# Kernel tuning notes

Hardware: AMD Instinct MI355X
Metric: run time of the kernel (lower is better)

The kernel has to match this reference:

```python
import jax, jax.numpy as jnp
import numpy as np

EPS_COS = 1e-8   # torch cosine_similarity eps
EPS_DEN = 1e-6   # denominator eps in original loss
TEMP = 0.1


def setup_inputs() -> dict:
    key = jax.random.key(0)
    k1, _ = jax.random.split(key)
    N, D = 16384, 2048
    x = jax.random.normal(k1, (N, D), dtype=jnp.float32)
    pos_pair = jnp.arange(2, dtype=jnp.int64)  # (i, j) = (0, 1), i != j
    return {"x": x, "pos_pair": pos_pair}


def reference(x, pos_pair):
    # x: [N, D]; pos_pair: [2] int indices (i, j)
    i = pos_pair[0]
    j = pos_pair[1]
    xi = x[i]                                        # [D] anchor
    # cosine similarity of anchor against every row (single fused matvec)
    dots = x @ xi                                    # [N]
    norms = jnp.maximum(jnp.linalg.norm(x, axis=1), EPS_COS)   # [N]
    ni = jnp.maximum(jnp.linalg.norm(xi), EPS_COS)
    cos = dots / (norms * ni)                        # [N]
    e = jnp.exp(cos / TEMP)                          # [N]
    # denominator sums over all k != i (k == j included, as in original)
    mask = jnp.arange(x.shape[0]) != i
    denominator = jnp.sum(jnp.where(mask, e, 0.0))
    nominator = e[j]
    loss = -jnp.log(nominator / (denominator + EPS_DEN))
    return loss.reshape(1)  # original returns shape [1]
```

## Files before the change

kernel.cpp:

```cpp
#include <hip/hip_runtime.h>
#include <math.h>

#define D 2048
#define EPS_COS 1e-8f
#define EPS_DEN 1e-6f
#define INV_TEMP 10.0f
#define TPB 256
#define WPB 4
#define NBLK 4096

__device__ __forceinline__ void get_ij(const int* __restrict__ p, int n,
                                       int& i, int& j) {
    int i32 = p[0], j32 = p[1];
    if (i32 >= 0 && i32 < n && j32 >= 0 && j32 < n && i32 != j32) {
        i = i32; j = j32; return;
    }
    const long long* p64 = (const long long*)p;
    i = (int)p64[0]; j = (int)p64[1];
}

__global__ __launch_bounds__(TPB)
void e_kernel(const float* __restrict__ x, const int* __restrict__ pos,
              float* __restrict__ part, float* __restrict__ nom, int n) {
    int i, j;
    get_ij(pos, n, i, j);
    const int lane = threadIdx.x & 63;
    const int wave = threadIdx.x >> 6;
    const int t    = threadIdx.x;
    const int row  = blockIdx.x * WPB + wave;

    const float4* __restrict__ xr = (const float4*)(x + (size_t)row * D);
    const float4* __restrict__ xi = (const float4*)(x + (size_t)i * D);

    __shared__ float4 s_xi[D / 4];
    __shared__ float  s_den[WPB];

    float4 x0 = xi[t];
    float4 x1 = xi[t + 256];

    float4 a[8];
#pragma unroll
    for (int w = 0; w < 8; ++w) a[w] = xr[lane + w * 64];

    s_xi[t]       = x0;
    s_xi[t + 256] = x1;
    __syncthreads();

    float dot = 0.f, sq = 0.f, sqi = 0.f;
#pragma unroll
    for (int w = 0; w < 8; ++w) {
        const float4 b = s_xi[lane + w * 64];
        dot = fmaf(a[w].x, b.x, fmaf(a[w].y, b.y,
              fmaf(a[w].z, b.z, fmaf(a[w].w, b.w, dot))));
        sq  = fmaf(a[w].x, a[w].x, fmaf(a[w].y, a[w].y,
              fmaf(a[w].z, a[w].z, fmaf(a[w].w, a[w].w, sq))));
        sqi = fmaf(b.x, b.x, fmaf(b.y, b.y,
              fmaf(b.z, b.z, fmaf(b.w, b.w, sqi))));
    }
#pragma unroll
    for (int off = 32; off; off >>= 1) {
        dot += __shfl_down(dot, off);
        sq  += __shfl_down(sq,  off);
        sqi += __shfl_down(sqi, off);
    }

    if (lane == 0) {
        float nk = fmaxf(sqrtf(sq),  EPS_COS);
        float ni = fmaxf(sqrtf(sqi), EPS_COS);
        float e  = expf(INV_TEMP * dot / (nk * ni));
        s_den[wave] = (row != i) ? e : 0.f;
        if (row == j) *nom = e;
    }
    __syncthreads();
    if (t == 0)
        part[blockIdx.x] = (s_den[0] + s_den[1]) + (s_den[2] + s_den[3]);
}

__global__ __launch_bounds__(1024)
void loss_kernel(const float* __restrict__ part, const float* __restrict__ nom,
                 float* __restrict__ out) {
    const int t = threadIdx.x;
    const float4 v = ((const float4*)part)[t];
    float s = (v.x + v.y) + (v.z + v.w);
#pragma unroll
    for (int off = 32; off; off >>= 1) s += __shfl_down(s, off);

    __shared__ float ls[16];
    if ((t & 63) == 0) ls[t >> 6] = s;
    __syncthreads();

    if (t == 0) {
        float den = 0.f;
#pragma unroll
        for (int w = 0; w < 16; ++w) den += ls[w];
        out[0] = -logf(nom[0] / (den + EPS_DEN));
    }
}

extern "C" void kernel_launch(void* const* d_in, const int* in_sizes, int n_in,
                              void* d_out, int out_size, void* d_ws, size_t ws_size,
                              hipStream_t stream) {
    const float* x    = (const float*)d_in[0];
    const int*   pos  = (const int*)d_in[1];
    float*       out  = (float*)d_out;
    float*       part = (float*)d_ws;
    float*       nom  = (float*)d_ws + NBLK;

    const int n = in_sizes[0] / D;

    e_kernel<<<NBLK, TPB, 0, stream>>>(x, pos, part, nom, n);
    loss_kernel<<<1, 1024, 0, stream>>>(part, nom, out);
}
```

Measured before the change: 187.2 us.

## Fuse similarity and loss reduction into one cooperative persistent kernel

Replaces the two-kernel launch with a single cooperative kernel of 1024 blocks. Each block processes four rows per wave in sequence, accumulates its denominator partial, then syncs the whole grid so block 0 can finish the reduction and write the loss. This removes the second kernel launch and amortizes the anchor-row load and anchor-norm computation across rows. The cost is the grid-wide barrier and less parallelism for hiding memory latency. It falls back to the old path if the cooperative launch fails.

```diff
diff --git a/kernel.cpp b/kernel.cpp
--- a/kernel.cpp
+++ b/kernel.cpp
@@ -1,5 +1,8 @@
 #include <hip/hip_runtime.h>
+#include <hip/hip_cooperative_groups.h>
 #include <math.h>
+
+namespace cg = cooperative_groups;
 
 #define D 2048
 #define EPS_COS 1e-8f
@@ -7,6 +10,8 @@
 #define INV_TEMP 10.0f
 #define TPB 256
 #define WPB 4
+#define FBLK 1024
+#define NPASS 4
 #define NBLK 4096
 
 __device__ __forceinline__ void get_ij(const int* __restrict__ p, int n,
@@ -17,6 +22,104 @@
     }
     const long long* p64 = (const long long*)p;
     i = (int)p64[0]; j = (int)p64[1];
+}
+
+__global__ __launch_bounds__(TPB, 4)
+void fused_kernel(const float* __restrict__ x, const int* __restrict__ pos,
+                  float* __restrict__ part, float* __restrict__ nom,
+                  float* __restrict__ out, int n) {
+    int i, j;
+    get_ij(pos, n, i, j);
+    const int lane = threadIdx.x & 63;
+    const int wave = threadIdx.x >> 6;
+    const int t    = threadIdx.x;
+    const int bid  = blockIdx.x;
+
+    __shared__ float4 s_xi[D / 4];
+    __shared__ float  s_red[WPB];
+
+    const float4* __restrict__ xi = (const float4*)(x + (size_t)i * D);
+    float4 x0 = xi[t];
+    float4 x1 = xi[t + 256];
+
+    const int row0 = bid * WPB + wave;
+    const float4* __restrict__ xr0 = (const float4*)(x + (size_t)row0 * D);
+    float4 a[8];
+#pragma unroll
+    for (int w = 0; w < 8; ++w) a[w] = xr0[lane + w * 64];
+
+    s_xi[t]       = x0;
+    s_xi[t + 256] = x1;
+    __syncthreads();
+
+    float den_acc = 0.f;
+    float ni_val  = 0.f;
+
+#pragma unroll
+    for (int p = 0; p < NPASS; ++p) {
+        const int row = p * (FBLK * WPB) + row0;
+        if (p > 0) {
+            const float4* __restrict__ xr =
+                (const float4*)(x + (size_t)row * D);
+#pragma unroll
+            for (int w = 0; w < 8; ++w) a[w] = xr[lane + w * 64];
+        }
+        float dot = 0.f, sq = 0.f, sqi = 0.f;
+#pragma unroll
+        for (int w = 0; w < 8; ++w) {
+            const float4 b = s_xi[lane + w * 64];
+            dot = fmaf(a[w].x, b.x, fmaf(a[w].y, b.y,
+                  fmaf(a[w].z, b.z, fmaf(a[w].w, b.w, dot))));
+            sq  = fmaf(a[w].x, a[w].x, fmaf(a[w].y, a[w].y,
+                  fmaf(a[w].z, a[w].z, fmaf(a[w].w, a[w].w, sq))));
+            if (p == 0)
+                sqi = fmaf(b.x, b.x, fmaf(b.y, b.y,
+                      fmaf(b.z, b.z, fmaf(b.w, b.w, sqi))));
+        }
+#pragma unroll
+        for (int off = 32; off; off >>= 1) {
+            dot += __shfl_down(dot, off);
+            sq  += __shfl_down(sq,  off);
+            if (p == 0) sqi += __shfl_down(sqi, off);
+        }
+        if (lane == 0) {
+            if (p == 0) ni_val = fmaxf(sqrtf(sqi), EPS_COS);
+            const float nk = fmaxf(sqrtf(sq), EPS_COS);
+            const float e  = expf(INV_TEMP * dot / (nk * ni_val));
+            if (row != i) den_acc += e;
+            if (row == j)
+                __hip_atomic_store(nom, e, __ATOMIC_RELAXED,
+                                   __HIP_MEMORY_SCOPE_AGENT);
+        }
+    }
+
+    if (lane == 0) s_red[wave] = den_acc;
+    __syncthreads();
+    if (t == 0) {
+        const float v = (s_red[0] + s_red[1]) + (s_red[2] + s_red[3]);
+        __hip_atomic_store(&part[bid], v, __ATOMIC_RELAXED,
+                           __HIP_MEMORY_SCOPE_AGENT);
+    }
+
+    cg::this_grid().sync();
+
+    if (bid == 0) {
+        float s = 0.f;
+#pragma unroll
+        for (int k = 0; k < FBLK / TPB; ++k)
+            s += __hip_atomic_load(&part[t + k * TPB], __ATOMIC_RELAXED,
+                                   __HIP_MEMORY_SCOPE_AGENT);
+#pragma unroll
+        for (int off = 32; off; off >>= 1) s += __shfl_down(s, off);
+        if (lane == 0) s_red[wave] = s;
+        __syncthreads();
+        if (t == 0) {
+            const float den = (s_red[0] + s_red[1]) + (s_red[2] + s_red[3]);
+            const float nm  = __hip_atomic_load(nom, __ATOMIC_RELAXED,
+                                                __HIP_MEMORY_SCOPE_AGENT);
+            out[0] = -logf(nm / (den + EPS_DEN));
+        }
+    }
 }
 
 __global__ __launch_bounds__(TPB)
@@ -105,9 +208,16 @@
     float*       out  = (float*)d_out;
     float*       part = (float*)d_ws;
     float*       nom  = (float*)d_ws + NBLK;
-
-    const int n = in_sizes[0] / D;
-
-    e_kernel<<<NBLK, TPB, 0, stream>>>(x, pos, part, nom, n);
-    loss_kernel<<<1, 1024, 0, stream>>>(part, nom, out);
-}
+    int          n    = in_sizes[0] / D;
+
+    void* args[6] = {(void*)&x, (void*)&pos, (void*)&part,
+                     (void*)&nom, (void*)&out, (void*)&n};
+    hipError_t err = hipLaunchCooperativeKernel(
+        reinterpret_cast<const void*>(&fused_kernel),
+        dim3(FBLK), dim3(TPB), args, 0, stream);
+
+    if (err != hipSuccess) {
+        e_kernel<<<NBLK, TPB, 0, stream>>>(x, pos, part, nom, n);
+        loss_kernel<<<1, 1024, 0, stream>>>(part, nom, out);
+    }
+}
```

Result: slower. 328.3 us (+75.4%).
